# Kernel optimization log

Hardware: AMD Instinct MI355X
Metric: run time of the kernel (lower is better)

Reference implementation:

```python
import jax, jax.numpy as jnp
import numpy as np
from jax import lax

ALPHA = 2.0        # elastic_alpha per axis
SMOOTH_NUM = 4
WIN = 5            # box smoothing window
FS = 11            # elastic field size per dim
SIZE_O = (128, 128, 128)


def _rodrigues(rot):
    # rot: (N,3) angle-axis -> (N,3,3) rotation matrix, with Taylor fallback near 0
    eps = 1e-6
    theta2 = jnp.sum(rot * rot, axis=1, keepdims=True)            # (N,1)
    theta = jnp.sqrt(jnp.maximum(theta2, eps))                    # safe sqrt
    w = rot / (theta + eps)
    wx, wy, wz = w[:, 0:1], w[:, 1:2], w[:, 2:3]
    c = jnp.cos(theta)
    s = jnp.sin(theta)
    k = 1.0 - c
    Rn = jnp.concatenate([
        c + wx * wx * k, wx * wy * k - wz * s, wy * s + wx * wz * k,
        wz * s + wx * wy * k, c + wy * wy * k, -wx * s + wy * wz * k,
        -wy * s + wx * wz * k, wx * s + wy * wz * k, c + wz * wz * k,
    ], axis=1).reshape(-1, 3, 3)
    rx, ry, rz = rot[:, 0:1], rot[:, 1:2], rot[:, 2:3]
    one = jnp.ones_like(rx)
    Rt = jnp.concatenate([one, -rz, ry, rz, one, -rx, -ry, rx, one],
                         axis=1).reshape(-1, 3, 3)
    mask = (theta2 > eps)[:, :, None]                             # (N,1,1)
    return jnp.where(mask, Rn, Rt)


def _box_smooth(d):
    # replicate-pad + mean box filter (torch __smooth_3d__)
    p = WIN // 2
    dp = jnp.pad(d, ((0, 0), (0, 0), (p, p), (p, p), (p, p)), mode='edge')
    k = jnp.ones((1, 1, WIN, WIN, WIN), d.dtype) / float(WIN ** 3)
    return lax.conv_general_dilated(dp, k, (1, 1, 1), 'VALID',
                                    dimension_numbers=('NCDHW', 'OIDHW', 'NCDHW'))


def _resize1d(x, axis, out_size):
    # linear interpolation along one axis, align_corners=False (torch interpolate)
    in_size = x.shape[axis]
    src = (jnp.arange(out_size, dtype=x.dtype) + 0.5) * (in_size / out_size) - 0.5
    src = jnp.clip(src, 0.0, in_size - 1.0)
    i0 = jnp.floor(src).astype(jnp.int32)
    i1 = jnp.minimum(i0 + 1, in_size - 1)
    w = (src - i0.astype(x.dtype))
    shape = [1] * x.ndim
    shape[axis] = out_size
    w = w.reshape(shape)
    x0 = jnp.take(x, i0, axis=axis)
    x1 = jnp.take(x, i1, axis=axis)
    return x0 * (1.0 - w) + x1 * w


def _resize3d(d, size):
    d = _resize1d(d, 2, size[0])
    d = _resize1d(d, 3, size[1])
    d = _resize1d(d, 4, size[2])
    return d


def _grid_sample3d(vol, grid):
    # vol: (N,C,D,H,W), grid: (N,D,H,W,3) normalized (x,y,z); trilinear, zeros pad,
    # align_corners=False (torch grid_sample defaults)
    N, C, D, H, W = vol.shape
    x = ((grid[..., 0] + 1.0) * W - 1.0) * 0.5
    y = ((grid[..., 1] + 1.0) * H - 1.0) * 0.5
    z = ((grid[..., 2] + 1.0) * D - 1.0) * 0.5
    x0f, y0f, z0f = jnp.floor(x), jnp.floor(y), jnp.floor(z)
    wx, wy, wz = x - x0f, y - y0f, z - z0f
    x0 = x0f.astype(jnp.int32)
    y0 = y0f.astype(jnp.int32)
    z0 = z0f.astype(jnp.int32)
    b = jnp.arange(N)[:, None, None, None]

    def gather(zi, yi, xi):
        valid = (zi >= 0) & (zi < D) & (yi >= 0) & (yi < H) & (xi >= 0) & (xi < W)
        v = vol[b, :, jnp.clip(zi, 0, D - 1), jnp.clip(yi, 0, H - 1),
                jnp.clip(xi, 0, W - 1)]                           # (N,Do,Ho,Wo,C)
        return v * valid[..., None].astype(vol.dtype)

    out = (gather(z0, y0, x0) * ((1 - wz) * (1 - wy) * (1 - wx))[..., None]
           + gather(z0, y0, x0 + 1) * ((1 - wz) * (1 - wy) * wx)[..., None]
           + gather(z0, y0 + 1, x0) * ((1 - wz) * wy * (1 - wx))[..., None]
           + gather(z0, y0 + 1, x0 + 1) * ((1 - wz) * wy * wx)[..., None]
           + gather(z0 + 1, y0, x0) * (wz * (1 - wy) * (1 - wx))[..., None]
           + gather(z0 + 1, y0, x0 + 1) * (wz * (1 - wy) * wx)[..., None]
           + gather(z0 + 1, y0 + 1, x0) * (wz * wy * (1 - wx))[..., None]
           + gather(z0 + 1, y0 + 1, x0 + 1) * (wz * wy * wx)[..., None])
    return jnp.transpose(out, (0, 4, 1, 2, 3))


def _field(raw, size):
    # raw uniform field -> scaled, smoothed, cropped, resized displacement (D,H,W)
    d = (raw - 0.5) * 2.0 * ALPHA
    for _ in range(SMOOTH_NUM):
        d = _box_smooth(d)
    p = WIN // 2
    d = d[:, :, p:p + FS, p:p + FS, p:p + FS]
    return _resize3d(d, size)[0, 0]


def _forward(vol, rot, scale, shift, dz, dy, dx):
    N, C, D, H, W = vol.shape
    R = _rodrigues(rot)                                  # (N,3,3)
    A = R * scale[:, None, :]                            # scale multiplies columns
    theta = jnp.concatenate([A, shift[:, :, None]], axis=2)  # (N,3,4)
    # base affine grid, align_corners=False: coord_i = (2i+1)/S - 1
    xs = (2.0 * jnp.arange(W, dtype=vol.dtype) + 1.0) / W - 1.0
    ys = (2.0 * jnp.arange(H, dtype=vol.dtype) + 1.0) / H - 1.0
    zs = (2.0 * jnp.arange(D, dtype=vol.dtype) + 1.0) / D - 1.0
    zz, yy, xx = jnp.meshgrid(zs, ys, xs, indexing='ij')
    pts = jnp.stack([xx, yy, zz, jnp.ones_like(xx)], axis=-1)    # (D,H,W,4)
    grid = jnp.einsum('nij,dhwj->ndhwi', theta, pts)             # (N,D,H,W,3)
    disp = jnp.stack([_field(dz, (D, H, W)), _field(dy, (D, H, W)),
                      _field(dx, (D, H, W))], axis=-1)           # (D,H,W,3)
    grid = grid + disp[None]
    out = _grid_sample3d(vol, grid)
    # central crop to SIZE_O
    zs0 = D // 2 - SIZE_O[0] // 2
    ys0 = H // 2 - SIZE_O[1] // 2
    xs0 = W // 2 - SIZE_O[2] // 2
    return out[:, :, zs0:zs0 + SIZE_O[0], ys0:ys0 + SIZE_O[1], xs0:xs0 + SIZE_O[2]]


def setup_inputs() -> dict:
    key = jax.random.key(0)
    k = jax.random.split(key, 7)
    vol = jax.random.normal(k[0], (4, 1, 160, 160, 160), dtype=jnp.float32)
    rot = (jax.random.uniform(k[1], (4, 3), dtype=jnp.float32) - 0.5) * 0.35   # ~±10 deg in rad
    scale = 0.9 + 0.2 * jax.random.uniform(k[2], (4, 3), dtype=jnp.float32)
    shift = (jax.random.uniform(k[3], (4, 3), dtype=jnp.float32) - 0.5) * 0.1
    dz = jax.random.uniform(k[4], (1, 1, 15, 15, 15), dtype=jnp.float32)
    dy = jax.random.uniform(k[5], (1, 1, 15, 15, 15), dtype=jnp.float32)
    dx = jax.random.uniform(k[6], (1, 1, 15, 15, 15), dtype=jnp.float32)
    return {"vol": vol, "rot": rot, "scale": scale, "shift": shift,
            "dz": dz, "dy": dy, "dx": dx}


def reference(vol, rot, scale, shift, dz, dy, dx):
    return _forward(vol, rot, scale, shift, dz, dy, dx)
```

## Files before the change

### kernel.cpp

```cpp
#include <hip/hip_runtime.h>
#include <hip/hip_bf16.h>

#define VD 160
#define OD 128
#define CROP0 16
#define FSZ 11
#define RAWSZ 15
#define NBATCH 4
#define ODQ 4

#define ESTR 17
#define EOH  (8*ESTR)
#define ECH  (8*8*ESTR)

__global__ __launch_bounds__(1024) void prep_kernel(
        const float* __restrict__ rot, const float* __restrict__ scale,
        const float* __restrict__ shift,
        const float* __restrict__ dz, const float* __restrict__ dy,
        const float* __restrict__ dx,
        float* __restrict__ theta, float* __restrict__ fields) {
    const int tid = threadIdx.x;
    const int chan = blockIdx.x;

    if (chan == 3) {
        int n = tid;
        if (n >= NBATCH) return;
        float rx = rot[n*3+0], ry = rot[n*3+1], rz = rot[n*3+2];
        float t2 = rx*rx + ry*ry + rz*rz;
        const float eps = 1e-6f;
        float th = sqrtf(fmaxf(t2, eps));
        float inv = 1.0f / (th + eps);
        float wx = rx*inv, wy = ry*inv, wz = rz*inv;
        float c = cosf(th), s = sinf(th), k = 1.0f - c;
        float R[9];
        if (t2 > eps) {
            R[0] = c + wx*wx*k;      R[1] = wx*wy*k - wz*s;  R[2] = wy*s + wx*wz*k;
            R[3] = wz*s + wx*wy*k;   R[4] = c + wy*wy*k;     R[5] = -wx*s + wy*wz*k;
            R[6] = -wy*s + wx*wz*k;  R[7] = wx*s + wy*wz*k;  R[8] = c + wz*wz*k;
        } else {
            R[0] = 1.0f; R[1] = -rz;  R[2] = ry;
            R[3] = rz;   R[4] = 1.0f; R[5] = -rx;
            R[6] = -ry;  R[7] = rx;   R[8] = 1.0f;
        }
        for (int i = 0; i < 3; ++i) {
            for (int j = 0; j < 3; ++j)
                theta[n*12 + i*4 + j] = R[i*3 + j] * scale[n*3 + j];
            theta[n*12 + i*4 + 3] = shift[n*3 + i];
        }
        return;
    }

    __shared__ float bufA[RAWSZ*RAWSZ*RAWSZ];
    __shared__ float bufB[RAWSZ*RAWSZ*RAWSZ];
    const float* raw = (chan == 0) ? dz : (chan == 1) ? dy : dx;
    const int NTOT = RAWSZ*RAWSZ*RAWSZ;

    for (int i = tid; i < NTOT; i += 1024)
        bufA[i] = (raw[i] - 0.5f) * 4.0f;

    int cz[4], cy[4], cxx[4];
    bool val[4];
    #pragma unroll
    for (int j = 0; j < 4; ++j) {
        const int i = tid + j*1024;
        val[j] = (i < NTOT);
        const int ii = val[j] ? i : 0;
        cz[j]  = ii / (RAWSZ*RAWSZ);
        const int r = ii % (RAWSZ*RAWSZ);
        cy[j]  = r / RAWSZ;
        cxx[j] = r % RAWSZ;
    }
    __syncthreads();

    float* src = bufA;
    float* dst = bufB;
    for (int it = 0; it < 4; ++it) {
        #pragma unroll
        for (int ax = 0; ax < 3; ++ax) {
            const int stride = (ax == 0) ? RAWSZ*RAWSZ : (ax == 1) ? RAWSZ : 1;
            #pragma unroll
            for (int j = 0; j < 4; ++j) {
                if (val[j]) {
                    const int i = tid + j*1024;
                    const int c = (ax == 0) ? cz[j] : (ax == 1) ? cy[j] : cxx[j];
                    const int ib = i - c*stride;
                    float s = 0.0f;
                    #pragma unroll
                    for (int t = -2; t <= 2; ++t) {
                        const int cc = min(max(c + t, 0), RAWSZ - 1);
                        s += src[ib + cc*stride];
                    }
                    dst[i] = s * 0.2f;
                }
            }
            __syncthreads();
            float* tmp = src; src = dst; dst = tmp;
        }
    }
    for (int i = tid; i < FSZ*FSZ*FSZ; i += 1024) {
        const int z = i / (FSZ*FSZ);
        const int r = i % (FSZ*FSZ);
        const int y = r / FSZ;
        const int x = r % FSZ;
        fields[chan*FSZ*FSZ*FSZ + i] =
            src[(z+2)*RAWSZ*RAWSZ + (y+2)*RAWSZ + (x+2)];
    }
}

__device__ __forceinline__ void resize_coord(int m, int& i0, int& i1, float& w) {
    float s = fmaf((float)m + 0.5f, (float)FSZ / (float)VD, -0.5f);
    s = fminf(fmaxf(s, 0.0f), (float)(FSZ - 1));
    float f = floorf(s);
    i0 = (int)f;
    i1 = min(i0 + 1, FSZ - 1);
    w = s - f;
}

__global__ __launch_bounds__(512) void sample_kernel(
        const float* __restrict__ vol, const float* __restrict__ theta,
        const float* __restrict__ fields, float* __restrict__ out) {
    __shared__ float e[3*ECH];

    const int tid  = threadIdx.x;
    const int lane = tid & 63;
    const int wl   = lane & 15;
    const int hl   = lane >> 4;
    const int wv   = tid >> 6;
    const int wx   = wv & 1;
    const int wh   = (wv >> 1) & 1;
    const int wd   = wv >> 2;

    const int ow_l = (wx << 4) | wl;
    const int oh_l = (wh << 2) | hl;
    const int ow   = (blockIdx.x << 5) | ow_l;
    const int oh   = (blockIdx.y << 3) | oh_l;
    const int odb  = (blockIdx.z & 15) << 3;
    const int n    = blockIdx.z >> 4;

    {
        const int xi   = tid & 15;
        const int row0 = tid >> 4;
        if (xi < FSZ) {
            const int eod  = row0 & 7;
            const int eoh0 = row0 >> 3;
            int zi0, zi1, yA0, yA1, yB0, yB1;
            float zw, ywA, ywB;
            resize_coord(odb + eod + CROP0, zi0, zi1, zw);
            const int hbase = (blockIdx.y << 3) + CROP0;
            resize_coord(hbase + eoh0,     yA0, yA1, ywA);
            resize_coord(hbase + eoh0 + 4, yB0, yB1, ywB);
            const float wz0 = 1.0f - zw;
            const float wA00 = wz0*(1.0f-ywA), wA01 = wz0*ywA;
            const float wA10 = zw*(1.0f-ywA),  wA11 = zw*ywA;
            const float wB00 = wz0*(1.0f-ywB), wB01 = wz0*ywB;
            const float wB10 = zw*(1.0f-ywB),  wB11 = zw*ywB;
            const int oA00 = zi0*121 + yA0*11 + xi, oA01 = zi0*121 + yA1*11 + xi;
            const int oA10 = zi1*121 + yA0*11 + xi, oA11 = zi1*121 + yA1*11 + xi;
            const int oB00 = zi0*121 + yB0*11 + xi, oB01 = zi0*121 + yB1*11 + xi;
            const int oB10 = zi1*121 + yB0*11 + xi, oB11 = zi1*121 + yB1*11 + xi;
            float* ew = &e[row0*ESTR + xi];
            #pragma unroll
            for (int i = 0; i < 6; ++i) {
                const float* f = fields + (i >> 1) * (FSZ*FSZ*FSZ);
                float v;
                if (i & 1)
                    v = f[oB00]*wB00 + f[oB01]*wB01 + f[oB10]*wB10 + f[oB11]*wB11;
                else
                    v = f[oA00]*wA00 + f[oA01]*wA01 + f[oA10]*wA10 + f[oA11]*wA11;
                ew[i * (32*ESTR)] = v * 80.0f;
            }
        }
    }
    __syncthreads();

    const int w_ = ow + CROP0;
    const int h_ = oh + CROP0;

    const float x = fmaf(2.0f * (float)w_ + 1.0f, 1.0f / (float)VD, -1.0f);
    const float y = fmaf(2.0f * (float)h_ + 1.0f, 1.0f / (float)VD, -1.0f);

    float s = fmaf((float)w_ + 0.5f, (float)FSZ / (float)VD, -0.5f);
    s = fminf(fmaxf(s, 0.0f), (float)(FSZ - 1));
    const float sf = floorf(s);
    const int   xi0 = (int)sf;
    const float xw  = s - sf;

    const float* th = theta + n*12;
    const float cx = fmaf(th[0]*x + th[1]*y + th[3], 80.0f, 79.5f);
    const float cy = fmaf(th[4]*x + th[5]*y + th[7], 80.0f, 79.5f);
    const float cz = fmaf(th[8]*x + th[9]*y + th[11], 80.0f, 79.5f);
    const float tz0 = th[2] * 80.0f, tz1 = th[6] * 80.0f, tz2 = th[10] * 80.0f;

    const float* v = vol + (size_t)n * (VD*VD*VD);

    const float* ebase = &e[oh_l*EOH + (wd << 2)*ESTR + xi0];

    const int dbase = odb + (wd << 2) + CROP0;
    const float zb = fmaf(2.0f * (float)dbase + 1.0f, 1.0f / (float)VD, -1.0f);
    float* op = out + ((((size_t)n*OD + (odb + (wd << 2)))*OD + oh)*OD + ow);

    #pragma unroll
    for (int k = 0; k < ODQ; ++k) {
        const float z = zb + (float)k * (2.0f / (float)VD);

        const float ex0 = ebase[        k*ESTR    ], ex1 = ebase[        k*ESTR + 1];
        const float ey0 = ebase[ECH   + k*ESTR    ], ey1 = ebase[ECH   + k*ESTR + 1];
        const float ez0 = ebase[2*ECH + k*ESTR    ], ez1 = ebase[2*ECH + k*ESTR + 1];
        const float d80x = fmaf(ex1 - ex0, xw, ex0);
        const float d80y = fmaf(ey1 - ey0, xw, ey0);
        const float d80z = fmaf(ez1 - ez0, xw, ez0);

        const float xs = fmaf(tz0, z, cx) + d80x;
        const float ys = fmaf(tz1, z, cy) + d80y;
        const float zs = fmaf(tz2, z, cz) + d80z;

        const float x0f = floorf(xs), y0f = floorf(ys), z0f = floorf(zs);
        const float fx = xs - x0f, fy = ys - y0f, fz = zs - z0f;
        const int ix0 = (int)x0f, iy0 = (int)y0f, iz0 = (int)z0f;

        float r;
        const int inb = ((unsigned)ix0 < (unsigned)(VD-1)) &
                        ((unsigned)iy0 < (unsigned)(VD-1)) &
                        ((unsigned)iz0 < (unsigned)(VD-1));
        if (__all(inb)) {
            const int b00 = (iz0*VD + iy0)*VD + ix0;
            float2 p00, p01, p10, p11;
            __builtin_memcpy(&p00, v + b00,             sizeof(float2));
            __builtin_memcpy(&p01, v + b00 + VD,        sizeof(float2));
            __builtin_memcpy(&p10, v + b00 + VD*VD,     sizeof(float2));
            __builtin_memcpy(&p11, v + b00 + VD*VD+VD,  sizeof(float2));
            const float r00 = fmaf(fx, p00.y - p00.x, p00.x);
            const float r01 = fmaf(fx, p01.y - p01.x, p01.x);
            const float r10 = fmaf(fx, p10.y - p10.x, p10.x);
            const float r11 = fmaf(fx, p11.y - p11.x, p11.x);
            const float r0 = fmaf(fy, r01 - r00, r00);
            const float r1 = fmaf(fy, r11 - r10, r10);
            r = fmaf(fz, r1 - r0, r0);
        } else {
            const int ix1 = ix0 + 1,  iy1 = iy0 + 1,  iz1 = iz0 + 1;

            const float WX0 = ((unsigned)ix0 < (unsigned)VD) ? (1.0f - fx) : 0.0f;
            const float WX1 = ((unsigned)ix1 < (unsigned)VD) ? fx          : 0.0f;
            const float WY0 = ((unsigned)iy0 < (unsigned)VD) ? (1.0f - fy) : 0.0f;
            const float WY1 = ((unsigned)iy1 < (unsigned)VD) ? fy          : 0.0f;
            const float WZ0 = ((unsigned)iz0 < (unsigned)VD) ? (1.0f - fz) : 0.0f;
            const float WZ1 = ((unsigned)iz1 < (unsigned)VD) ? fz          : 0.0f;

            const int xc0 = min(max(ix0, 0), VD-1), xc1 = min(max(ix1, 0), VD-1);
            const int yc0 = min(max(iy0, 0), VD-1), yc1 = min(max(iy1, 0), VD-1);
            const int zc0 = min(max(iz0, 0), VD-1), zc1 = min(max(iz1, 0), VD-1);

            const int base = min(xc0, VD-2);
            const bool hi0 = (xc0 != base);
            const bool hi1 = (xc1 != base);
            const float wA = (hi0 ? 0.0f : WX0) + (hi1 ? 0.0f : WX1);
            const float wB = (hi0 ? WX0 : 0.0f) + (hi1 ? WX1 : 0.0f);

            const int sA = zc0*(VD*VD), sB = zc1*(VD*VD);
            const int tA = yc0*VD + base, tB = yc1*VD + base;

            float2 p00, p01, p10, p11;
            __builtin_memcpy(&p00, v + sA + tA, sizeof(float2));
            __builtin_memcpy(&p01, v + sA + tB, sizeof(float2));
            __builtin_memcpy(&p10, v + sB + tA, sizeof(float2));
            __builtin_memcpy(&p11, v + sB + tB, sizeof(float2));

            const float r00 = p00.x*wA + p00.y*wB;
            const float r01 = p01.x*wA + p01.y*wB;
            const float r10 = p10.x*wA + p10.y*wB;
            const float r11 = p11.x*wA + p11.y*wB;
            r = (r00*WY0 + r01*WY1)*WZ0 + (r10*WY0 + r11*WY1)*WZ1;
        }

        op[(size_t)k*OD*OD] = r;
    }
}

extern "C" void kernel_launch(void* const* d_in, const int* in_sizes, int n_in,
                              void* d_out, int out_size, void* d_ws, size_t ws_size,
                              hipStream_t stream) {
    const float* vol   = (const float*)d_in[0];
    const float* rot   = (const float*)d_in[1];
    const float* scale = (const float*)d_in[2];
    const float* shift = (const float*)d_in[3];
    const float* dz    = (const float*)d_in[4];
    const float* dy    = (const float*)d_in[5];
    const float* dx    = (const float*)d_in[6];
    float* out = (float*)d_out;

    float* ws     = (float*)d_ws;
    float* theta  = ws;
    float* fields = ws + 48;

    prep_kernel<<<4, 1024, 0, stream>>>(rot, scale, shift, dz, dy, dx,
                                        theta, fields);
    dim3 grid(OD/32, OD/8, (OD/8)*NBATCH);
    sample_kernel<<<grid, 512, 0, stream>>>(vol, theta, fields, out);
}
```

Before: 145.0 us.

## Precompute smoothing as matrix, batch gathers across depth, add nontemporal stores

The repeated 1D box-smoothing passes in the prep kernel are replaced by a compile-time 15x15 matrix for four smoothing passes. It is applied once per axis, computing only the 11 cropped outputs. In the sample kernel, all four depth samples are computed first with a single wave-wide in-bounds test, so their gathers can be issued together. Stores become nontemporal, the barrier moves later, and launch bounds request higher occupancy. This raises register pressure, and one out-of-bounds sample now sends all four samples down the slow path.

```diff
diff --git a/kernel.cpp b/kernel.cpp
--- a/kernel.cpp
+++ b/kernel.cpp
@@ -1,5 +1,4 @@
 #include <hip/hip_runtime.h>
-#include <hip/hip_bf16.h>
 
 #define VD 160
 #define OD 128
@@ -12,6 +11,31 @@
 #define ESTR 17
 #define EOH  (8*ESTR)
 #define ECH  (8*8*ESTR)
+
+struct M15 { float v[15][15]; };
+constexpr M15 mkB() {
+    M15 b{};
+    for (int i = 0; i < 15; ++i)
+        for (int j = 0; j < 15; ++j) b.v[i][j] = 0.0f;
+    for (int i = 0; i < 15; ++i)
+        for (int t = -2; t <= 2; ++t) {
+            int j = i + t; j = j < 0 ? 0 : (j > 14 ? 14 : j);
+            b.v[i][j] += 0.2f;
+        }
+    return b;
+}
+constexpr M15 mmul(const M15& a, const M15& b) {
+    M15 c{};
+    for (int i = 0; i < 15; ++i)
+        for (int j = 0; j < 15; ++j) {
+            float s = 0.0f;
+            for (int k = 0; k < 15; ++k) s += a.v[i][k] * b.v[k][j];
+            c.v[i][j] = s;
+        }
+    return c;
+}
+constexpr M15 B2 = mmul(mkB(), mkB());
+constexpr M15 B4 = mmul(B2, B2);
 
 __global__ __launch_bounds__(1024) void prep_kernel(
         const float* __restrict__ rot, const float* __restrict__ scale,
@@ -51,59 +75,50 @@
     }
 
     __shared__ float bufA[RAWSZ*RAWSZ*RAWSZ];
-    __shared__ float bufB[RAWSZ*RAWSZ*RAWSZ];
+    __shared__ float bufB[RAWSZ*RAWSZ*FSZ];
+    __shared__ float bufC[RAWSZ*FSZ*FSZ];
     const float* raw = (chan == 0) ? dz : (chan == 1) ? dy : dx;
     const int NTOT = RAWSZ*RAWSZ*RAWSZ;
 
     for (int i = tid; i < NTOT; i += 1024)
         bufA[i] = (raw[i] - 0.5f) * 4.0f;
-
-    int cz[4], cy[4], cxx[4];
-    bool val[4];
-    #pragma unroll
-    for (int j = 0; j < 4; ++j) {
-        const int i = tid + j*1024;
-        val[j] = (i < NTOT);
-        const int ii = val[j] ? i : 0;
-        cz[j]  = ii / (RAWSZ*RAWSZ);
-        const int r = ii % (RAWSZ*RAWSZ);
-        cy[j]  = r / RAWSZ;
-        cxx[j] = r % RAWSZ;
-    }
     __syncthreads();
 
-    float* src = bufA;
-    float* dst = bufB;
-    for (int it = 0; it < 4; ++it) {
-        #pragma unroll
-        for (int ax = 0; ax < 3; ++ax) {
-            const int stride = (ax == 0) ? RAWSZ*RAWSZ : (ax == 1) ? RAWSZ : 1;
-            #pragma unroll
-            for (int j = 0; j < 4; ++j) {
-                if (val[j]) {
-                    const int i = tid + j*1024;
-                    const int c = (ax == 0) ? cz[j] : (ax == 1) ? cy[j] : cxx[j];
-                    const int ib = i - c*stride;
-                    float s = 0.0f;
-                    #pragma unroll
-                    for (int t = -2; t <= 2; ++t) {
-                        const int cc = min(max(c + t, 0), RAWSZ - 1);
-                        s += src[ib + cc*stride];
-                    }
-                    dst[i] = s * 0.2f;
-                }
-            }
-            __syncthreads();
-            float* tmp = src; src = dst; dst = tmp;
-        }
-    }
+    for (int i = tid; i < RAWSZ*RAWSZ*FSZ; i += 1024) {
+        const int zy = i / FSZ;
+        const int xo = i % FSZ;
+        const float* row = &bufA[zy * RAWSZ];
+        const float* w = B4.v[xo + 2];
+        float s = 0.0f;
+        #pragma unroll
+        for (int j = 0; j < RAWSZ; ++j) s += row[j] * w[j];
+        bufB[i] = s;
+    }
+    __syncthreads();
+
+    for (int i = tid; i < RAWSZ*FSZ*FSZ; i += 1024) {
+        const int z  = i / (FSZ*FSZ);
+        const int r  = i % (FSZ*FSZ);
+        const int yo = r / FSZ;
+        const int xo = r % FSZ;
+        const float* base = &bufB[z * (RAWSZ*FSZ) + xo];
+        const float* w = B4.v[yo + 2];
+        float s = 0.0f;
+        #pragma unroll
+        for (int j = 0; j < RAWSZ; ++j) s += base[j * FSZ] * w[j];
+        bufC[i] = s;
+    }
+    __syncthreads();
+
     for (int i = tid; i < FSZ*FSZ*FSZ; i += 1024) {
-        const int z = i / (FSZ*FSZ);
-        const int r = i % (FSZ*FSZ);
-        const int y = r / FSZ;
-        const int x = r % FSZ;
-        fields[chan*FSZ*FSZ*FSZ + i] =
-            src[(z+2)*RAWSZ*RAWSZ + (y+2)*RAWSZ + (x+2)];
+        const int zo = i / (FSZ*FSZ);
+        const int r  = i % (FSZ*FSZ);
+        const float* base = &bufC[r];
+        const float* w = B4.v[zo + 2];
+        float s = 0.0f;
+        #pragma unroll
+        for (int j = 0; j < RAWSZ; ++j) s += base[j * (FSZ*FSZ)] * w[j];
+        fields[chan*FSZ*FSZ*FSZ + i] = s;
     }
 }
 
@@ -116,7 +131,7 @@
     w = s - f;
 }
 
-__global__ __launch_bounds__(512) void sample_kernel(
+__global__ __launch_bounds__(512, 4) void sample_kernel(
         const float* __restrict__ vol, const float* __restrict__ theta,
         const float* __restrict__ fields, float* __restrict__ out) {
     __shared__ float e[3*ECH];
@@ -171,7 +186,6 @@
             }
         }
     }
-    __syncthreads();
 
     const int w_ = ow + CROP0;
     const int h_ = oh + CROP0;
@@ -199,56 +213,72 @@
     const float zb = fmaf(2.0f * (float)dbase + 1.0f, 1.0f / (float)VD, -1.0f);
     float* op = out + ((((size_t)n*OD + (odb + (wd << 2)))*OD + oh)*OD + ow);
 
+    __syncthreads();
+
+    float ex0[ODQ], ex1[ODQ], ey0[ODQ], ey1[ODQ], ez0[ODQ], ez1[ODQ];
+    #pragma unroll
+    for (int k = 0; k < ODQ; ++k) {
+        ex0[k] = ebase[        k*ESTR    ];  ex1[k] = ebase[        k*ESTR + 1];
+        ey0[k] = ebase[ECH   + k*ESTR    ];  ey1[k] = ebase[ECH   + k*ESTR + 1];
+        ez0[k] = ebase[2*ECH + k*ESTR    ];  ez1[k] = ebase[2*ECH + k*ESTR + 1];
+    }
+
+    float fx[ODQ], fy[ODQ], fz[ODQ];
+    int ix[ODQ], iy[ODQ], iz[ODQ];
+    int inb = 1;
     #pragma unroll
     for (int k = 0; k < ODQ; ++k) {
         const float z = zb + (float)k * (2.0f / (float)VD);
-
-        const float ex0 = ebase[        k*ESTR    ], ex1 = ebase[        k*ESTR + 1];
-        const float ey0 = ebase[ECH   + k*ESTR    ], ey1 = ebase[ECH   + k*ESTR + 1];
-        const float ez0 = ebase[2*ECH + k*ESTR    ], ez1 = ebase[2*ECH + k*ESTR + 1];
-        const float d80x = fmaf(ex1 - ex0, xw, ex0);
-        const float d80y = fmaf(ey1 - ey0, xw, ey0);
-        const float d80z = fmaf(ez1 - ez0, xw, ez0);
-
+        const float d80x = fmaf(ex1[k] - ex0[k], xw, ex0[k]);
+        const float d80y = fmaf(ey1[k] - ey0[k], xw, ey0[k]);
+        const float d80z = fmaf(ez1[k] - ez0[k], xw, ez0[k]);
         const float xs = fmaf(tz0, z, cx) + d80x;
         const float ys = fmaf(tz1, z, cy) + d80y;
         const float zs = fmaf(tz2, z, cz) + d80z;
-
         const float x0f = floorf(xs), y0f = floorf(ys), z0f = floorf(zs);
-        const float fx = xs - x0f, fy = ys - y0f, fz = zs - z0f;
-        const int ix0 = (int)x0f, iy0 = (int)y0f, iz0 = (int)z0f;
-
-        float r;
-        const int inb = ((unsigned)ix0 < (unsigned)(VD-1)) &
-                        ((unsigned)iy0 < (unsigned)(VD-1)) &
-                        ((unsigned)iz0 < (unsigned)(VD-1));
-        if (__all(inb)) {
-            const int b00 = (iz0*VD + iy0)*VD + ix0;
-            float2 p00, p01, p10, p11;
-            __builtin_memcpy(&p00, v + b00,             sizeof(float2));
-            __builtin_memcpy(&p01, v + b00 + VD,        sizeof(float2));
-            __builtin_memcpy(&p10, v + b00 + VD*VD,     sizeof(float2));
-            __builtin_memcpy(&p11, v + b00 + VD*VD+VD,  sizeof(float2));
-            const float r00 = fmaf(fx, p00.y - p00.x, p00.x);
-            const float r01 = fmaf(fx, p01.y - p01.x, p01.x);
-            const float r10 = fmaf(fx, p10.y - p10.x, p10.x);
-            const float r11 = fmaf(fx, p11.y - p11.x, p11.x);
-            const float r0 = fmaf(fy, r01 - r00, r00);
-            const float r1 = fmaf(fy, r11 - r10, r10);
-            r = fmaf(fz, r1 - r0, r0);
-        } else {
-            const int ix1 = ix0 + 1,  iy1 = iy0 + 1,  iz1 = iz0 + 1;
-
-            const float WX0 = ((unsigned)ix0 < (unsigned)VD) ? (1.0f - fx) : 0.0f;
-            const float WX1 = ((unsigned)ix1 < (unsigned)VD) ? fx          : 0.0f;
-            const float WY0 = ((unsigned)iy0 < (unsigned)VD) ? (1.0f - fy) : 0.0f;
-            const float WY1 = ((unsigned)iy1 < (unsigned)VD) ? fy          : 0.0f;
-            const float WZ0 = ((unsigned)iz0 < (unsigned)VD) ? (1.0f - fz) : 0.0f;
-            const float WZ1 = ((unsigned)iz1 < (unsigned)VD) ? fz          : 0.0f;
-
-            const int xc0 = min(max(ix0, 0), VD-1), xc1 = min(max(ix1, 0), VD-1);
-            const int yc0 = min(max(iy0, 0), VD-1), yc1 = min(max(iy1, 0), VD-1);
-            const int zc0 = min(max(iz0, 0), VD-1), zc1 = min(max(iz1, 0), VD-1);
+        fx[k] = xs - x0f; fy[k] = ys - y0f; fz[k] = zs - z0f;
+        ix[k] = (int)x0f; iy[k] = (int)y0f; iz[k] = (int)z0f;
+        inb &= ((unsigned)ix[k] < (unsigned)(VD-1)) &
+               ((unsigned)iy[k] < (unsigned)(VD-1)) &
+               ((unsigned)iz[k] < (unsigned)(VD-1));
+    }
+
+    if (__all(inb)) {
+        float2 p00[ODQ], p01[ODQ], p10[ODQ], p11[ODQ];
+        #pragma unroll
+        for (int k = 0; k < ODQ; ++k) {
+            const int b00 = (iz[k]*VD + iy[k])*VD + ix[k];
+            __builtin_memcpy(&p00[k], v + b00,            sizeof(float2));
+            __builtin_memcpy(&p01[k], v + b00 + VD,       sizeof(float2));
+            __builtin_memcpy(&p10[k], v + b00 + VD*VD,    sizeof(float2));
+            __builtin_memcpy(&p11[k], v + b00 + VD*VD+VD, sizeof(float2));
+        }
+        #pragma unroll
+        for (int k = 0; k < ODQ; ++k) {
+            const float r00 = fmaf(fx[k], p00[k].y - p00[k].x, p00[k].x);
+            const float r01 = fmaf(fx[k], p01[k].y - p01[k].x, p01[k].x);
+            const float r10 = fmaf(fx[k], p10[k].y - p10[k].x, p10[k].x);
+            const float r11 = fmaf(fx[k], p11[k].y - p11[k].x, p11[k].x);
+            const float r0 = fmaf(fy[k], r01 - r00, r00);
+            const float r1 = fmaf(fy[k], r11 - r10, r10);
+            const float r  = fmaf(fz[k], r1 - r0, r0);
+            __builtin_nontemporal_store(r, op + (size_t)k*OD*OD);
+        }
+    } else {
+        #pragma unroll
+        for (int k = 0; k < ODQ; ++k) {
+            const int ix1 = ix[k] + 1, iy1 = iy[k] + 1, iz1 = iz[k] + 1;
+
+            const float WX0 = ((unsigned)ix[k] < (unsigned)VD) ? (1.0f - fx[k]) : 0.0f;
+            const float WX1 = ((unsigned)ix1   < (unsigned)VD) ? fx[k]          : 0.0f;
+            const float WY0 = ((unsigned)iy[k] < (unsigned)VD) ? (1.0f - fy[k]) : 0.0f;
+            const float WY1 = ((unsigned)iy1   < (unsigned)VD) ? fy[k]          : 0.0f;
+            const float WZ0 = ((unsigned)iz[k] < (unsigned)VD) ? (1.0f - fz[k]) : 0.0f;
+            const float WZ1 = ((unsigned)iz1   < (unsigned)VD) ? fz[k]          : 0.0f;
+
+            const int xc0 = min(max(ix[k], 0), VD-1), xc1 = min(max(ix1, 0), VD-1);
+            const int yc0 = min(max(iy[k], 0), VD-1), yc1 = min(max(iy1, 0), VD-1);
+            const int zc0 = min(max(iz[k], 0), VD-1), zc1 = min(max(iz1, 0), VD-1);
 
             const int base = min(xc0, VD-2);
             const bool hi0 = (xc0 != base);
@@ -269,10 +299,10 @@
             const float r01 = p01.x*wA + p01.y*wB;
             const float r10 = p10.x*wA + p10.y*wB;
             const float r11 = p11.x*wA + p11.y*wB;
-            r = (r00*WY0 + r01*WY1)*WZ0 + (r10*WY0 + r11*WY1)*WZ1;
-        }
-
-        op[(size_t)k*OD*OD] = r;
+            const float r = (r00*WY0 + r01*WY1)*WZ0 + (r10*WY0 + r11*WY1)*WZ1;
+
+            __builtin_nontemporal_store(r, op + (size_t)k*OD*OD);
+        }
     }
 }
 
```

New measurement: 143.6 us. Within noise of the previous version (-1.0%).
